# Kernel tuning notes

Measured on AMD Instinct MI355X. Metric: run time of the kernel, lower is better.

The kernel has to match this reference:

```python
import jax, jax.numpy as jnp
import numpy as np

N_EMBD = 1024
N_HEAD = 64

def setup_inputs() -> dict:
    key = jax.random.key(0)
    ks = jax.random.split(key, 7)
    B, T = 4, 4096
    x = jax.random.normal(ks[0], (B, T, N_EMBD), dtype=jnp.float32)
    # causal mask: True above the diagonal (masked positions)
    mask = jnp.triu(jnp.ones((T, T), dtype=bool), k=1)
    s = 1.0 / np.sqrt(N_EMBD)
    Wq = jax.random.normal(ks[1], (N_EMBD, N_HEAD), dtype=jnp.float32) * s
    bq = jnp.zeros((N_HEAD,), dtype=jnp.float32)
    Wk = jax.random.normal(ks[2], (N_EMBD, N_HEAD), dtype=jnp.float32) * s
    bk = jnp.zeros((N_HEAD,), dtype=jnp.float32)
    Wv = jax.random.normal(ks[3], (N_EMBD, N_HEAD), dtype=jnp.float32) * s
    bv = jnp.zeros((N_HEAD,), dtype=jnp.float32)
    return {"x": x, "mask": mask, "Wq": Wq, "bq": bq, "Wk": Wk, "bk": bk, "Wv": Wv, "bv": bv}

def reference(x, mask, Wq, bq, Wk, bk, Wv, bv):
    # x: [B,T,C], mask: [T,T] bool (True = masked)
    q = x @ Wq + bq            # [B,T,H]
    k = x @ Wk + bk            # [B,T,H]
    v = x @ Wv + bv            # [B,T,H]
    scale = 1.0 / jnp.sqrt(jnp.asarray(q.shape[-1], dtype=q.dtype))
    att = jnp.einsum('bth,bsh->bts', q, k) * scale   # [B,T,T]
    att = jnp.where(mask[None, :, :], -jnp.inf, att)
    att = jax.nn.softmax(att, axis=-1)
    # dropout omitted (eval mode / deterministic reference)
    return jnp.einsum('bts,bsh->bth', att, v)        # [B,T,H]
```

## Files before the change

kernel.cpp:

```cpp
#include <hip/hip_runtime.h>
#include <hip/hip_bf16.h>

#define BB 4
#define TT 4096
#define CC 1024
#define HH 64

#define QSCALE 0.18033688011112042f
#define FIXMAX2 23.083120654223414f

typedef __attribute__((ext_vector_type(8))) short short8;
typedef __attribute__((ext_vector_type(4))) float floatx4;

__device__ __forceinline__ ushort f2bf(float f) {
    union { float f; unsigned u; } a; a.f = f;
    const unsigned u = a.u;
    return (ushort)((u + 0x7fffu + ((u >> 16) & 1u)) >> 16);
}
__device__ __forceinline__ float bf2f(ushort h) {
    union { unsigned u; float f; } a; a.u = ((unsigned)h) << 16; return a.f;
}

__global__ __launch_bounds__(256)
void wtrans_kernel(const float* __restrict__ Wq, const float* __restrict__ Wk,
                   const float* __restrict__ Wv, ushort* __restrict__ wT)
{
    __shared__ ushort tile[64 * 72];
    const int tid = threadIdx.x;
    const int mat = blockIdx.x >> 4, kt = blockIdx.x & 15;
    const float* W = (mat == 0) ? Wq : (mat == 1) ? Wk : Wv;
    #pragma unroll
    for (int it = 0; it < 16; ++it) {
        const int idx = it * 256 + tid;
        const int r = idx >> 6, c = idx & 63;
        tile[c * 72 + r] = f2bf(W[(size_t)(kt * 64 + r) * 64 + c]);
    }
    __syncthreads();
    #pragma unroll
    for (int it = 0; it < 16; ++it) {
        const int idx = it * 256 + tid;
        const int n = idx >> 6, kk = idx & 63;
        wT[((size_t)mat * 64 + n) * 1024 + kt * 64 + kk] = tile[n * 72 + kk];
    }
}

__global__ __launch_bounds__(256)
void qkv_mfma_kernel(const float* __restrict__ x, const ushort* __restrict__ wT,
                     const float* __restrict__ bq, const float* __restrict__ bk,
                     const float* __restrict__ bv,
                     ushort* __restrict__ q, ushort* __restrict__ k,
                     ushort* __restrict__ vT)
{
    __shared__ ushort xs [16 * 72];
    __shared__ ushort ws_[192 * 72];

    const int tid = threadIdx.x, w = tid >> 6, lane = tid & 63;
    const int m = lane & 15, quad = lane >> 4;
    const int row0 = blockIdx.x * 16;

    floatx4 acc[3];
    #pragma unroll
    for (int i = 0; i < 3; ++i) acc[i] = (floatx4){0.f, 0.f, 0.f, 0.f};

    for (int kc = 0; kc < 16; ++kc) {
        const int k0 = kc * 64;
        __syncthreads();
        {
            const int r = tid >> 4, seg = tid & 15;
            const float4 f0 = *(const float4*)(x + (size_t)(row0 + r) * CC + k0 + seg * 4);
            ushort4 p;
            p.x = f2bf(f0.x); p.y = f2bf(f0.y); p.z = f2bf(f0.z); p.w = f2bf(f0.w);
            *(ushort4*)(xs + r * 72 + seg * 4) = p;
        }
        #pragma unroll
        for (int it = 0; it < 6; ++it) {
            const int idx = it * 256 + tid;
            const int r = idx >> 3, g = idx & 7;
            *(uint4*)(ws_ + r * 72 + g * 8) =
                *(const uint4*)(wT + (size_t)r * 1024 + k0 + g * 8);
        }
        __syncthreads();

        #pragma unroll
        for (int ks_ = 0; ks_ < 2; ++ks_) {
            const short8 a = *(const short8*)(xs + m * 72 + ks_ * 32 + quad * 8);
            #pragma unroll
            for (int j = 0; j < 3; ++j) {
                const short8 b_ = *(const short8*)(ws_ + (w * 48 + j * 16 + m) * 72 + ks_ * 32 + quad * 8);
                acc[j] = __builtin_amdgcn_mfma_f32_16x16x32_bf16(a, b_, acc[j], 0, 0, 0);
            }
        }
    }

    const int gr0 = row0 + quad * 4;
    const int b_ = gr0 >> 12, t0 = gr0 & (TT - 1);
    #pragma unroll
    for (int j = 0; j < 3; ++j) {
        const int nt = w * 3 + j;
        const int mat = nt >> 2;
        const int c = (nt & 3) * 16 + m;
        const float bias = (mat == 0) ? bq[c] : (mat == 1) ? bk[c] : bv[c];
        if (mat == 0) {
            #pragma unroll
            for (int r = 0; r < 4; ++r)
                q[(size_t)(gr0 + r) * HH + c] = f2bf((acc[j][r] + bias) * QSCALE);
        } else if (mat == 1) {
            #pragma unroll
            for (int r = 0; r < 4; ++r)
                k[(size_t)(gr0 + r) * HH + c] = f2bf(acc[j][r] + bias);
        } else {
            ushort4 pv;
            pv.x = f2bf(acc[j][0] + bias); pv.y = f2bf(acc[j][1] + bias);
            pv.z = f2bf(acc[j][2] + bias); pv.w = f2bf(acc[j][3] + bias);
            *(ushort4*)(vT + ((size_t)b_ * HH + c) * TT + t0) = pv;
        }
    }
}

__global__ __launch_bounds__(256)
void attn_mfma_kernel(const ushort* __restrict__ q, const ushort* __restrict__ k,
                      const ushort* __restrict__ vT,
                      float* __restrict__ partL, ushort* __restrict__ partO)
{
    __shared__ ushort ks[64 * 72];
    __shared__ ushort vs[64 * 72];
    __shared__ ushort ps[4][16 * 72];

    const int tid = threadIdx.x, w = tid >> 6, lane = tid & 63;
    const int m = lane & 15, quad = lane >> 4;
    const int pid = blockIdx.x;
    const int job = pid >> 3, split = pid & 7;
    const int b = job >> 6, tile = job & 63;
    const int i0 = tile * 64;
    const int nch = tile + 1;
    const int lo = (nch * split) >> 3, hi = (nch * (split + 1)) >> 3;

    const size_t qrow = ((size_t)b * TT + i0 + w * 16 + m) * HH;
    const uint4 aq0u = *(const uint4*)(q + qrow + quad * 8);
    const uint4 aq1u = *(const uint4*)(q + qrow + 32 + quad * 8);
    const short8 aq0 = *(const short8*)&aq0u;
    const short8 aq1 = *(const short8*)&aq1u;

    float lrow[4] = {0.f, 0.f, 0.f, 0.f};
    floatx4 oacc[4];
    #pragma unroll
    for (int nt = 0; nt < 4; ++nt) oacc[nt] = (floatx4){0.f, 0.f, 0.f, 0.f};

    const int iq0 = i0 + w * 16;
    for (int ch = lo; ch < hi; ++ch) {
        const int s0 = ch * 64;
        __syncthreads();
        const size_t kb = ((size_t)b * TT + s0) * HH;
        #pragma unroll
        for (int it = 0; it < 2; ++it) {
            const int t2 = it * 256 + tid;
            const int r = t2 >> 3, seg = t2 & 7;
            *(uint4*)(ks + r * 72 + seg * 8) = *(const uint4*)(k + kb + (size_t)r * HH + seg * 8);
            *(uint4*)(vs + r * 72 + seg * 8) = *(const uint4*)(vT + ((size_t)b * HH + r) * TT + s0 + seg * 8);
        }
        __syncthreads();

        floatx4 sc[4];
        #pragma unroll
        for (int nt = 0; nt < 4; ++nt) {
            const short8 b0 = *(const short8*)(ks + (nt * 16 + m) * 72 + quad * 8);
            const short8 b1 = *(const short8*)(ks + (nt * 16 + m) * 72 + 32 + quad * 8);
            floatx4 s_ = (floatx4){0.f, 0.f, 0.f, 0.f};
            s_ = __builtin_amdgcn_mfma_f32_16x16x32_bf16(aq0, b0, s_, 0, 0, 0);
            s_ = __builtin_amdgcn_mfma_f32_16x16x32_bf16(aq1, b1, s_, 0, 0, 0);
            sc[nt] = s_;
        }

        const bool need_mask = (s0 + 63 > iq0);
        #pragma unroll
        for (int r = 0; r < 4; ++r) {
            float t0 = sc[0][r] - FIXMAX2;
            float t1 = sc[1][r] - FIXMAX2;
            float t2 = sc[2][r] - FIXMAX2;
            float t3 = sc[3][r] - FIXMAX2;
            if (need_mask) {
                const int dlim = iq0 + quad * 4 + r - s0 - m;
                if (0  > dlim) t0 = -1e30f;
                if (16 > dlim) t1 = -1e30f;
                if (32 > dlim) t2 = -1e30f;
                if (48 > dlim) t3 = -1e30f;
            }
            const float p0 = __builtin_amdgcn_exp2f(t0);
            const float p1 = __builtin_amdgcn_exp2f(t1);
            const float p2 = __builtin_amdgcn_exp2f(t2);
            const float p3 = __builtin_amdgcn_exp2f(t3);
            lrow[r] += (p0 + p1) + (p2 + p3);
            ushort* pr = ps[w] + (quad * 4 + r) * 72;
            pr[m]      = f2bf(p0);
            pr[16 + m] = f2bf(p1);
            pr[32 + m] = f2bf(p2);
            pr[48 + m] = f2bf(p3);
        }

        #pragma unroll
        for (int ks_ = 0; ks_ < 2; ++ks_) {
            const short8 ap = *(const short8*)(ps[w] + m * 72 + ks_ * 32 + quad * 8);
            #pragma unroll
            for (int nt = 0; nt < 4; ++nt) {
                const short8 bv_ = *(const short8*)(vs + (nt * 16 + m) * 72 + ks_ * 32 + quad * 8);
                oacc[nt] = __builtin_amdgcn_mfma_f32_16x16x32_bf16(ap, bv_, oacc[nt], 0, 0, 0);
            }
        }
    }

    #pragma unroll
    for (int r = 0; r < 4; ++r) {
        float s = lrow[r];
        s += __shfl_xor(s, 1); s += __shfl_xor(s, 2);
        s += __shfl_xor(s, 4); s += __shfl_xor(s, 8);
        lrow[r] = s;
    }
    if (m == 0) {
        #pragma unroll
        for (int r = 0; r < 4; ++r)
            partL[(size_t)pid * 64 + w * 16 + quad * 4 + r] = lrow[r];
    }
    ushort* po = partO + ((size_t)pid * 64 + w * 16) * 64;
    #pragma unroll
    for (int r = 0; r < 4; ++r) {
        const int row = quad * 4 + r;
        #pragma unroll
        for (int nt = 0; nt < 4; ++nt)
            po[row * 64 + nt * 16 + m] = f2bf(oacc[nt][r]);
    }
}

__global__ __launch_bounds__(256)
void attn_combine_kernel(const float* __restrict__ partL,
                         const ushort* __restrict__ partO, float* __restrict__ out)
{
    const int job = blockIdx.x;
    const int tid = threadIdx.x;
    const int row = tid >> 2, dq = tid & 3;

    float L = 0.f;
    #pragma unroll
    for (int s = 0; s < 8; ++s) L += partL[(size_t)(job * 8 + s) * 64 + row];
    const float inv = 1.f / L;

    float o[16];
    #pragma unroll
    for (int i = 0; i < 16; ++i) o[i] = 0.f;
    #pragma unroll
    for (int s = 0; s < 8; ++s) {
        const ushort* po = partO + (((size_t)(job * 8 + s) * 64 + row) * 64 + dq * 16);
        #pragma unroll
        for (int i2 = 0; i2 < 2; ++i2) {
            const ushort4 pa = *(const ushort4*)(po + i2 * 8);
            const ushort4 pb = *(const ushort4*)(po + i2 * 8 + 4);
            o[i2*8+0] += bf2f(pa.x); o[i2*8+1] += bf2f(pa.y);
            o[i2*8+2] += bf2f(pa.z); o[i2*8+3] += bf2f(pa.w);
            o[i2*8+4] += bf2f(pb.x); o[i2*8+5] += bf2f(pb.y);
            o[i2*8+6] += bf2f(pb.z); o[i2*8+7] += bf2f(pb.w);
        }
    }
    float4* dst = (float4*)(out + ((size_t)job * 64 + row) * 64 + dq * 16);
    #pragma unroll
    for (int i = 0; i < 4; ++i) {
        float4 v; v.x = o[i*4]*inv; v.y = o[i*4+1]*inv; v.z = o[i*4+2]*inv; v.w = o[i*4+3]*inv;
        dst[i] = v;
    }
}

extern "C" void kernel_launch(void* const* d_in, const int* in_sizes, int n_in,
                              void* d_out, int out_size, void* d_ws, size_t ws_size,
                              hipStream_t stream) {
    (void)in_sizes; (void)n_in; (void)out_size; (void)ws_size;
    const float* x  = (const float*)d_in[0];
    const float* Wq = (const float*)d_in[2];
    const float* bq = (const float*)d_in[3];
    const float* Wk = (const float*)d_in[4];
    const float* bk = (const float*)d_in[5];
    const float* Wv = (const float*)d_in[6];
    const float* bv = (const float*)d_in[7];
    float* out = (float*)d_out;

    char* ws = (char*)d_ws;
    ushort* wT    = (ushort*)ws;
    ushort* qb    = (ushort*)(ws + 393216);
    ushort* kb    = qb + (size_t)BB * TT * HH;
    ushort* vTb   = kb + (size_t)BB * TT * HH;
    float*  partL = (float*) (ws + 6684672);
    ushort* partO = (ushort*)(ws + 7208960);

    wtrans_kernel   <<<48, 256, 0, stream>>>(Wq, Wk, Wv, wT);
    qkv_mfma_kernel <<<(BB * TT) / 16, 256, 0, stream>>>(x, wT, bq, bk, bv, qb, kb, vTb);
    attn_mfma_kernel<<<BB * 64 * 8, 256, 0, stream>>>(qb, kb, vTb, partL, partO);
    attn_combine_kernel<<<BB * 64, 256, 0, stream>>>(partL, partO, out);
}
```

Baseline: 206.7 us.

## Prefetch next K-chunk into registers and double rows per QKV projection block

The QKV projection kernel now loads the next 64-wide K chunk of x and the transposed weights into registers while the MFMAs for the current chunk run, hiding global load latency. Blocks grow to 512 threads covering 32 rows, so each weight tile staged in shared memory is reused by twice as many rows, halving redundant weight traffic. Block count halves to 512, which may reduce latency hiding across CUs, and register pressure rises from the prefetch buffers.

```diff
diff --git a/kernel.cpp b/kernel.cpp
--- a/kernel.cpp
+++ b/kernel.cpp
@@ -44,59 +44,80 @@
     }
 }
 
-__global__ __launch_bounds__(256)
+__global__ __launch_bounds__(512)
 void qkv_mfma_kernel(const float* __restrict__ x, const ushort* __restrict__ wT,
                      const float* __restrict__ bq, const float* __restrict__ bk,
                      const float* __restrict__ bv,
                      ushort* __restrict__ q, ushort* __restrict__ k,
                      ushort* __restrict__ vT)
 {
-    __shared__ ushort xs [16 * 72];
+    __shared__ ushort xs [32 * 72];
     __shared__ ushort ws_[192 * 72];
 
     const int tid = threadIdx.x, w = tid >> 6, lane = tid & 63;
     const int m = lane & 15, quad = lane >> 4;
-    const int row0 = blockIdx.x * 16;
+    const int mt = w >> 2, colq = w & 3;
+    const int row0 = blockIdx.x * 32;
 
     floatx4 acc[3];
     #pragma unroll
     for (int i = 0; i < 3; ++i) acc[i] = (floatx4){0.f, 0.f, 0.f, 0.f};
 
+    const int xr = tid >> 4, xseg = tid & 15;
+
+    float4 pfx;
+    uint4  pfw[3];
+    {
+        pfx = *(const float4*)(x + (size_t)(row0 + xr) * CC + xseg * 4);
+        #pragma unroll
+        for (int it = 0; it < 3; ++it) {
+            const int idx = it * 512 + tid;
+            const int r = idx >> 3, g = idx & 7;
+            pfw[it] = *(const uint4*)(wT + (size_t)r * 1024 + g * 8);
+        }
+    }
+
     for (int kc = 0; kc < 16; ++kc) {
-        const int k0 = kc * 64;
         __syncthreads();
         {
-            const int r = tid >> 4, seg = tid & 15;
-            const float4 f0 = *(const float4*)(x + (size_t)(row0 + r) * CC + k0 + seg * 4);
             ushort4 p;
-            p.x = f2bf(f0.x); p.y = f2bf(f0.y); p.z = f2bf(f0.z); p.w = f2bf(f0.w);
-            *(ushort4*)(xs + r * 72 + seg * 4) = p;
-        }
-        #pragma unroll
-        for (int it = 0; it < 6; ++it) {
-            const int idx = it * 256 + tid;
-            const int r = idx >> 3, g = idx & 7;
-            *(uint4*)(ws_ + r * 72 + g * 8) =
-                *(const uint4*)(wT + (size_t)r * 1024 + k0 + g * 8);
+            p.x = f2bf(pfx.x); p.y = f2bf(pfx.y); p.z = f2bf(pfx.z); p.w = f2bf(pfx.w);
+            *(ushort4*)(xs + xr * 72 + xseg * 4) = p;
+            #pragma unroll
+            for (int it = 0; it < 3; ++it) {
+                const int idx = it * 512 + tid;
+                const int r = idx >> 3, g = idx & 7;
+                *(uint4*)(ws_ + r * 72 + g * 8) = pfw[it];
+            }
         }
         __syncthreads();
+        if (kc + 1 < 16) {
+            const int k0 = (kc + 1) * 64;
+            pfx = *(const float4*)(x + (size_t)(row0 + xr) * CC + k0 + xseg * 4);
+            #pragma unroll
+            for (int it = 0; it < 3; ++it) {
+                const int idx = it * 512 + tid;
+                const int r = idx >> 3, g = idx & 7;
+                pfw[it] = *(const uint4*)(wT + (size_t)r * 1024 + k0 + g * 8);
+            }
+        }
 
         #pragma unroll
         for (int ks_ = 0; ks_ < 2; ++ks_) {
-            const short8 a = *(const short8*)(xs + m * 72 + ks_ * 32 + quad * 8);
+            const short8 a = *(const short8*)(xs + (mt * 16 + m) * 72 + ks_ * 32 + quad * 8);
             #pragma unroll
             for (int j = 0; j < 3; ++j) {
-                const short8 b_ = *(const short8*)(ws_ + (w * 48 + j * 16 + m) * 72 + ks_ * 32 + quad * 8);
+                const short8 b_ = *(const short8*)(ws_ + ((colq * 3 + j) * 16 + m) * 72 + ks_ * 32 + quad * 8);
                 acc[j] = __builtin_amdgcn_mfma_f32_16x16x32_bf16(a, b_, acc[j], 0, 0, 0);
             }
         }
     }
 
-    const int gr0 = row0 + quad * 4;
+    const int gr0 = row0 + mt * 16 + quad * 4;
     const int b_ = gr0 >> 12, t0 = gr0 & (TT - 1);
     #pragma unroll
     for (int j = 0; j < 3; ++j) {
-        const int nt = w * 3 + j;
+        const int nt = colq * 3 + j;
         const int mat = nt >> 2;
         const int c = (nt & 3) * 16 + m;
         const float bias = (mat == 0) ? bq[c] : (mat == 1) ? bk[c] : bv[c];
@@ -289,7 +310,7 @@
     ushort* partO = (ushort*)(ws + 7208960);
 
     wtrans_kernel   <<<48, 256, 0, stream>>>(Wq, Wk, Wv, wT);
-    qkv_mfma_kernel <<<(BB * TT) / 16, 256, 0, stream>>>(x, wT, bq, bk, bv, qb, kb, vTb);
+    qkv_mfma_kernel <<<(BB * TT) / 32, 512, 0, stream>>>(x, wT, bq, bk, bv, qb, kb, vTb);
     attn_mfma_kernel<<<BB * 64 * 8, 256, 0, stream>>>(qb, kb, vTb, partL, partO);
     attn_combine_kernel<<<BB * 64, 256, 0, stream>>>(partL, partO, out);
 }
```

New measurement: 240.2 us. 16.2% more time.
